# Kernel optimization log

Hardware: AMD Instinct MI355X
Metric: run time of the kernel (lower is better)

## Reference

```python
import jax, jax.numpy as jnp
import numpy as np

N = 50000   # nodes
E = 1000000 # edges
D = 64      # input_nf = output_nf = hidden_nf
COORDS_WEIGHT = 1.0


def setup_inputs() -> dict:
    key = jax.random.key(0)
    ks = jax.random.split(key, 16)
    h = jax.random.normal(ks[0], (N, D), dtype=jnp.float32)
    coord = jax.random.normal(ks[1], (N, 3), dtype=jnp.float32)
    edge_index = jax.random.randint(ks[2], (2, E), 0, N, dtype=jnp.int32)
    s = 0.05  # generic init scale
    # edge_mlp: Linear(2D+1 -> D), ReLU, Linear(D -> D), ReLU
    We1 = jax.random.normal(ks[3], (2 * D + 1, D), dtype=jnp.float32) * s
    be1 = jnp.zeros((D,), dtype=jnp.float32)
    We2 = jax.random.normal(ks[4], (D, D), dtype=jnp.float32) * s
    be2 = jnp.zeros((D,), dtype=jnp.float32)
    # node_mlp: Linear(2D -> D), ReLU, Linear(D -> D)
    Wn1 = jax.random.normal(ks[5], (2 * D, D), dtype=jnp.float32) * s
    bn1 = jnp.zeros((D,), dtype=jnp.float32)
    Wn2 = jax.random.normal(ks[6], (D, D), dtype=jnp.float32) * s
    bn2 = jnp.zeros((D,), dtype=jnp.float32)
    # coord_mlp: Linear(D -> D), ReLU, Linear(D -> 1, no bias, xavier gain 0.001)
    Wc1 = jax.random.normal(ks[7], (D, D), dtype=jnp.float32) * s
    bc1 = jnp.zeros((D,), dtype=jnp.float32)
    Wc2 = jax.random.normal(ks[8], (D, 1), dtype=jnp.float32) * 0.001
    return {"h": h, "coord": coord, "edge_index": edge_index,
            "We1": We1, "be1": be1, "We2": We2, "be2": be2,
            "Wn1": Wn1, "bn1": bn1, "Wn2": Wn2, "bn2": bn2,
            "Wc1": Wc1, "bc1": bc1, "Wc2": Wc2}


def reference(h, coord, edge_index, We1, be1, We2, be2, Wn1, bn1, Wn2, bn2, Wc1, bc1, Wc2):
    row, col = edge_index[0], edge_index[1]
    # coord2radial (no PBC offsets; plain pairwise difference)
    coord_diff = coord[row] - coord[col]                    # [E, 3]
    radial = jnp.sum(coord_diff ** 2, axis=1, keepdims=True)  # [E, 1]

    # edge model: MLP on [h_i, h_j, ||x_i - x_j||^2]
    e_in = jnp.concatenate([h[row], h[col], radial], axis=1)  # [E, 2D+1]
    m = jax.nn.relu(e_in @ We1 + be1)
    edge_feat = jax.nn.relu(m @ We2 + be2)                   # [E, D]

    # coord model: per-edge scalar gate, clamp, segment mean
    gate = jax.nn.relu(edge_feat @ Wc1 + bc1) @ Wc2          # [E, 1]
    trans = jnp.clip(coord_diff * gate, -100.0, 100.0)       # [E, 3]
    trans_sum = jax.ops.segment_sum(trans, row, num_segments=N)  # [N, 3]
    cnt = jax.ops.segment_sum(jnp.ones((row.shape[0],), dtype=trans.dtype), row, num_segments=N)
    coord_out = (trans_sum / jnp.maximum(cnt, 1.0)[:, None]) * COORDS_WEIGHT  # [N, 3]

    # node model: scatter-sum aggregate then MLP with residual
    agg = jax.ops.segment_sum(edge_feat, row, num_segments=N)  # [N, D]
    n_in = jnp.concatenate([h, agg], axis=1)                   # [N, 2D]
    h_out = h + (jax.nn.relu(n_in @ Wn1 + bn1) @ Wn2 + bn2)    # residual
    return (h_out, coord_out)
```

## Files before the change

kernel.cpp:

```cpp
#include <hip/hip_runtime.h>

typedef float  f32x4  __attribute__((ext_vector_type(4)));
typedef __bf16 bf16x8 __attribute__((ext_vector_type(8)));
typedef unsigned short u16x8 __attribute__((ext_vector_type(8)));
typedef unsigned int   u32x4 __attribute__((ext_vector_type(4)));

__device__ inline unsigned short f2b(float f) {
    unsigned u = __builtin_bit_cast(unsigned, f);
    u += 0x7fffu + ((u >> 16) & 1u);
    return (unsigned short)(u >> 16);
}

__device__ inline unsigned pk2(float a, float b) {
    return (unsigned)f2b(a) | ((unsigned)f2b(b) << 16);
}

__device__ inline f32x4 mfma16(bf16x8 a, bf16x8 b, f32x4 c) {
    return __builtin_amdgcn_mfma_f32_16x16x32_bf16(a, b, c, 0, 0, 0);
}

__device__ inline bf16x8 cvt8(f32x4 a, f32x4 b) {
    u16x8 v;
    v[0] = f2b(a[0]); v[1] = f2b(a[1]); v[2] = f2b(a[2]); v[3] = f2b(a[3]);
    v[4] = f2b(b[0]); v[5] = f2b(b[1]); v[6] = f2b(b[2]); v[7] = f2b(b[3]);
    return __builtin_bit_cast(bf16x8, v);
}

__device__ inline bf16x8 ldsA(const unsigned short* base, int frag, int lane) {
    return __builtin_bit_cast(bf16x8,
        *reinterpret_cast<const u16x8*>(base + ((frag * 64 + lane) << 3)));
}

__device__ inline void atom_pk(unsigned short* p, unsigned d) {
    asm volatile("global_atomic_pk_add_bf16 %0, %1, off" :: "v"(p), "v"(d) : "memory");
}

__global__ void k_hist(const int* __restrict__ erow, int* __restrict__ cnt, int E)
{
    int i = blockIdx.x * 256 + threadIdx.x;
    if (i < E) atomicAdd(&cnt[erow[i]], 1);
}

__global__ void k_scan1(const int* __restrict__ cnt, int* __restrict__ bsum, int N)
{
    const int b = blockIdx.x, t = threadIdx.x;
    const int chunk = (N + gridDim.x - 1) / gridDim.x;
    const int lo = b * chunk;
    const int hi = min(lo + chunk, N);
    int s = 0;
    for (int i = lo + t; i < hi; i += 256) s += cnt[i];
#pragma unroll
    for (int d = 1; d < 64; d <<= 1) s += __shfl_xor(s, d, 64);
    __shared__ int ws[4];
    if ((t & 63) == 0) ws[t >> 6] = s;
    __syncthreads();
    if (t == 0) bsum[b] = ws[0] + ws[1] + ws[2] + ws[3];
}

__global__ void k_scan2(int* __restrict__ bsum)
{
    __shared__ int wt[2];
    const int t = threadIdx.x;
    const int lane = t & 63;
    int v = bsum[t];
    int sc = v;
#pragma unroll
    for (int d = 1; d < 64; d <<= 1) { int u = __shfl_up(sc, d, 64); if (lane >= d) sc += u; }
    if (lane == 63) wt[t >> 6] = sc;
    __syncthreads();
    int add = (t >= 64) ? wt[0] : 0;
    bsum[t] = sc - v + add;
}

__global__ void k_scan3(const int* __restrict__ cnt, const int* __restrict__ bsum,
                        int* __restrict__ off, int* __restrict__ woff, int N, int E)
{
    const int b = blockIdx.x, t = threadIdx.x;
    const int chunk = (N + gridDim.x - 1) / gridDim.x;
    const int lo = b * chunk;
    const int hi = min(lo + chunk, N);
    const int tchunk = (chunk + 255) / 256;
    const int tlo = lo + t * tchunk;
    const int thi = min(tlo + tchunk, hi);
    int s = 0;
    for (int i = tlo; i < thi; ++i) s += cnt[i];
    const int lane = t & 63, wv = t >> 6;
    int sc = s;
#pragma unroll
    for (int d = 1; d < 64; d <<= 1) { int u = __shfl_up(sc, d, 64); if (lane >= d) sc += u; }
    __shared__ int ws[4];
    if (lane == 63) ws[wv] = sc;
    __syncthreads();
    int wadd = 0;
#pragma unroll
    for (int k = 0; k < 4; ++k) wadd += (k < wv) ? ws[k] : 0;
    int run = bsum[b] + wadd + (sc - s);
    for (int i = tlo; i < thi; ++i) { off[i] = run; woff[i] = run; run += cnt[i]; }
    if (b == 0 && t == 0) off[N] = E;
}

__global__ void k_scatter(const int* __restrict__ erow, const int* __restrict__ ecol,
                          int* __restrict__ woff, unsigned* __restrict__ spack, int E)
{
    int i = blockIdx.x * 256 + threadIdx.x;
    if (i < E) {
        int r = erow[i];
        int pos = atomicAdd(&woff[r], 1);
        spack[pos] = (unsigned)r | ((unsigned)ecol[i] << 16);
    }
}

__global__ __launch_bounds__(512, 2) void egcl_edge_srt(
    const unsigned short* __restrict__ hb,
    const float* __restrict__ coord,
    const unsigned* __restrict__ spack,
    const float* __restrict__ We1, const float* __restrict__ be1,
    const float* __restrict__ We2, const float* __restrict__ be2,
    const float* __restrict__ Wc1, const float* __restrict__ bc1,
    const float* __restrict__ Wc2,
    unsigned short* __restrict__ aggb, float* __restrict__ cacc, int E)
{
    __shared__ __align__(16) unsigned short A1[16 * 512];
    __shared__ __align__(16) unsigned short A2[8 * 512];
    __shared__ __align__(16) unsigned short A3[8 * 512];
    __shared__ __align__(16) float bv[5][64];
    __shared__ __align__(16) unsigned stl[8][34 * 16];

    const int t = threadIdx.x;
    for (int i = t; i < 8192; i += 512) {
        int j = i & 7, lane = (i >> 3) & 63, fi = i >> 9;
        int mt = fi >> 2, ks = fi & 3;
        int in_ch = ks * 32 + ((lane >> 4) << 3) + j;
        int out   = mt * 16 + (lane & 15);
        A1[i] = f2b(We1[in_ch * 64 + out]);
    }
    for (int i = t; i < 4096; i += 512) {
        int j = i & 7, lane = (i >> 3) & 63, fi = i >> 9;
        int mt = fi >> 1, ks = fi & 1;
        int c   = (ks * 2 + (j >> 2)) * 16 + ((lane >> 4) & 3) * 4 + (j & 3);
        int out = mt * 16 + (lane & 15);
        A2[i] = f2b(We2[c * 64 + out]);
        A3[i] = f2b(Wc1[c * 64 + out]);
    }
    if (t < 64) {
        bv[0][t] = be1[t]; bv[1][t] = We1[128 * 64 + t];
        bv[2][t] = be2[t]; bv[3][t] = bc1[t]; bv[4][t] = Wc2[t];
    }
    __syncthreads();

    const int lane = t & 63;
    const int l16 = lane & 15, lq = lane >> 4;
    const int stride = gridDim.x * 8;
    const int wid = (blockIdx.x << 3) + (t >> 6);
    const int ntile = E >> 4;
    const int last = ntile - 1;
    unsigned* st = stl[t >> 6];

    int tile = wid;
    if (tile >= ntile) return;

    int eC = (tile << 4) + l16;
    unsigned pC = spack[eC];
    int rC = (int)(pC & 0xffffu), cC = (int)(pC >> 16);
    u16x8 hr0, hr1, hc0, hc1;
    {
        const u16x8* hr = reinterpret_cast<const u16x8*>(hb + (size_t)rC * 64);
        const u16x8* hc = reinterpret_cast<const u16x8*>(hb + (size_t)cC * 64);
        hr0 = hr[lq]; hr1 = hr[4 + lq]; hc0 = hc[lq]; hc1 = hc[4 + lq];
    }
    float px = 0.f, py = 0.f, pz = 0.f;
    if (lq < 2) {
        int node = (lq == 0) ? rC : cC;
        const float* pp = coord + (size_t)node * 3;
        px = pp[0]; py = pp[1]; pz = pp[2];
    }
    int t1 = tile + stride;
    int tn = (t1 < ntile) ? t1 : last;
    unsigned pN = spack[(tn << 4) + l16];
    int rN = (int)(pN & 0xffffu), cN = (int)(pN >> 16);

    for (; tile < ntile; ) {
        u16x8 nr0, nr1, nc0, nc1;
        {
            const u16x8* hr = reinterpret_cast<const u16x8*>(hb + (size_t)rN * 64);
            const u16x8* hc = reinterpret_cast<const u16x8*>(hb + (size_t)cN * 64);
            nr0 = hr[lq]; nr1 = hr[4 + lq]; nc0 = hc[lq]; nc1 = hc[4 + lq];
        }
        float npx = 0.f, npy = 0.f, npz = 0.f;
        if (lq < 2) {
            int node = (lq == 0) ? rN : cN;
            const float* pp = coord + (size_t)node * 3;
            npx = pp[0]; npy = pp[1]; npz = pp[2];
        }
        int t2 = tile + 2 * stride;
        int t2c = (t2 < ntile) ? t2 : last;
        unsigned pNN = spack[(t2c << 4) + l16];
        int rNN = (int)(pNN & 0xffffu), cNN = (int)(pNN >> 16);

        float prx = __shfl(px, l16, 64), pry = __shfl(py, l16, 64), prz = __shfl(pz, l16, 64);
        float pcx = __shfl(px, 16 + l16, 64), pcy = __shfl(py, 16 + l16, 64), pcz = __shfl(pz, 16 + l16, 64);
        float dx = prx - pcx, dy = pry - pcy, dz = prz - pcz;
        float rad = dx * dx + dy * dy + dz * dz;

        bf16x8 bR[2] = { __builtin_bit_cast(bf16x8, hr0), __builtin_bit_cast(bf16x8, hr1) };
        bf16x8 bC[2] = { __builtin_bit_cast(bf16x8, hc0), __builtin_bit_cast(bf16x8, hc1) };

        f32x4 a1[4];
#pragma unroll
        for (int mt = 0; mt < 4; ++mt)
            a1[mt] = *reinterpret_cast<const f32x4*>(&bv[0][mt * 16 + lq * 4]);
#pragma unroll
        for (int ks = 0; ks < 2; ++ks)
#pragma unroll
            for (int mt = 0; mt < 4; ++mt)
                a1[mt] = mfma16(ldsA(A1, mt * 4 + ks, lane), bR[ks], a1[mt]);
#pragma unroll
        for (int ks = 0; ks < 2; ++ks)
#pragma unroll
            for (int mt = 0; mt < 4; ++mt)
                a1[mt] = mfma16(ldsA(A1, mt * 4 + 2 + ks, lane), bC[ks], a1[mt]);
#pragma unroll
        for (int mt = 0; mt < 4; ++mt) {
            f32x4 wv = *reinterpret_cast<const f32x4*>(&bv[1][mt * 16 + lq * 4]);
#pragma unroll
            for (int rr = 0; rr < 4; ++rr)
                a1[mt][rr] = fmaxf(a1[mt][rr] + rad * wv[rr], 0.f);
        }

        bf16x8 b2[2] = { cvt8(a1[0], a1[1]), cvt8(a1[2], a1[3]) };
        f32x4 a2[4];
#pragma unroll
        for (int mt = 0; mt < 4; ++mt)
            a2[mt] = *reinterpret_cast<const f32x4*>(&bv[2][mt * 16 + lq * 4]);
#pragma unroll
        for (int ks = 0; ks < 2; ++ks)
#pragma unroll
            for (int mt = 0; mt < 4; ++mt)
                a2[mt] = mfma16(ldsA(A2, mt * 2 + ks, lane), b2[ks], a2[mt]);
#pragma unroll
        for (int mt = 0; mt < 4; ++mt)
#pragma unroll
            for (int rr = 0; rr < 4; ++rr)
                a2[mt][rr] = fmaxf(a2[mt][rr], 0.f);

#pragma unroll
        for (int mt = 0; mt < 4; ++mt) {
            int cp0 = mt * 8 + lq * 2;
            int sw  = l16 ^ (cp0 & 12);
            st[(cp0 + 0) * 16 + sw] = pk2(a2[mt][0], a2[mt][1]);
            st[(cp0 + 1) * 16 + sw] = pk2(a2[mt][2], a2[mt][3]);
        }

        bf16x8 b3[2] = { cvt8(a2[0], a2[1]), cvt8(a2[2], a2[3]) };
        f32x4 a3[4];
#pragma unroll
        for (int mt = 0; mt < 4; ++mt)
            a3[mt] = *reinterpret_cast<const f32x4*>(&bv[3][mt * 16 + lq * 4]);
#pragma unroll
        for (int ks = 0; ks < 2; ++ks)
#pragma unroll
            for (int mt = 0; mt < 4; ++mt)
                a3[mt] = mfma16(ldsA(A3, mt * 2 + ks, lane), b3[ks], a3[mt]);
        float gg = 0.f;
#pragma unroll
        for (int mt = 0; mt < 4; ++mt) {
            f32x4 wv = *reinterpret_cast<const f32x4*>(&bv[4][mt * 16 + lq * 4]);
#pragma unroll
            for (int rr = 0; rr < 4; ++rr)
                gg += fmaxf(a3[mt][rr], 0.f) * wv[rr];
        }
        gg += __shfl_xor(gg, 16, 64);
        gg += __shfl_xor(gg, 32, 64);

        float dsel = (lq == 0) ? dx : (lq == 1) ? dy : dz;
        float val  = fminf(fmaxf(dsel * gg, -100.f), 100.f);

        float vy = __shfl(val, 16 + l16, 64);
        if (lq == 0) st[32 * 16 + l16] = pk2(val, vy);
        if (lq == 2) st[33 * 16 + l16] = pk2(val, 1.0f);

        u16x8 sv;
#pragma unroll
        for (int j = 0; j < 8; ++j) {
            int ks = lq * 8 + j;
            int rk = __shfl(rC, ks & 15, 64);
            sv[j] = (ks < 16 && rk == rC) ? (unsigned short)0x3F80 : (unsigned short)0;
        }
        bf16x8 self = __builtin_bit_cast(bf16x8, sv);

        f32x4 pg[5];
#pragma unroll
        for (int k = 0; k < 5; ++k) pg[k] = (f32x4){0.f, 0.f, 0.f, 0.f};
        const int elo = (lq & 1) << 3;
#pragma unroll
        for (int tt = 0; tt < 5; ++tt) {
            int cpb = (tt < 4) ? (tt * 8 + (l16 >> 1)) : (32 + ((l16 >> 1) & 1));
            int c   = cpb & 12;
            u32x4 wa = *reinterpret_cast<const u32x4*>(st + cpb * 16 + (elo ^ c));
            u32x4 wb = *reinterpret_cast<const u32x4*>(st + cpb * 16 + ((elo + 4) ^ c));
            u16x8 av;
#pragma unroll
            for (int j = 0; j < 4; ++j) {
                av[j]     = (l16 & 1) ? (unsigned short)(wa[j] >> 16)
                                      : (unsigned short)(wa[j] & 0xffffu);
                av[4 + j] = (l16 & 1) ? (unsigned short)(wb[j] >> 16)
                                      : (unsigned short)(wb[j] & 0xffffu);
            }
            pg[tt] = mfma16(__builtin_bit_cast(bf16x8, av), self, pg[tt]);
        }

#pragma unroll
        for (int mt = 0; mt < 4; ++mt) {
            int cp0 = mt * 8 + lq * 2;
            int sw  = l16 ^ (cp0 & 12);
            st[(cp0 + 0) * 16 + sw] = pk2(pg[mt][0], pg[mt][1]);
            st[(cp0 + 1) * 16 + sw] = pk2(pg[mt][2], pg[mt][3]);
        }

        int rprev = __shfl(rC, (lane & 48) | ((l16 + 15) & 15), 64);
        bool lead = (l16 == 0) || (rprev != rC);

        if (lead && lq == 0) {
#pragma unroll
            for (int rr = 0; rr < 4; ++rr)
                atomicAdd(&cacc[(size_t)rC * 4 + rr], pg[4][rr]);
        }

        {
            unsigned m = (unsigned)(__ballot(lead) & 0xFFFFull);
            const int cp = lane & 31;
            const int half = lane >> 5;
            while (m) {
                int s0 = __builtin_ctz(m); m &= m - 1;
                int s1 = 16;
                if (m) { s1 = __builtin_ctz(m); m &= m - 1; }
                int s = half ? s1 : s0;
                if (s < 16) {
                    int rw = __shfl(rC, s, 64);
                    unsigned pkd = st[cp * 16 + (s ^ (cp & 12))];
                    atom_pk(aggb + (size_t)rw * 64 + cp * 2, pkd);
                }
            }
        }

        tile = t1; t1 = tile + stride;
        rC = rN; cC = cN; rN = rNN; cN = cNN;
        hr0 = nr0; hr1 = nr1; hc0 = nc0; hc1 = nc1;
        px = npx; py = npy; pz = npz;
    }
}

__global__ __launch_bounds__(512, 4) void egcl_edge_fb(
    const float* __restrict__ h, const float* __restrict__ coord,
    const int* __restrict__ erow, const int* __restrict__ ecol,
    const float* __restrict__ We1, const float* __restrict__ be1,
    const float* __restrict__ We2, const float* __restrict__ be2,
    const float* __restrict__ Wc1, const float* __restrict__ bc1,
    const float* __restrict__ Wc2,
    float* __restrict__ aggf, float* __restrict__ cacc, int E)
{
    __shared__ __align__(16) unsigned short A1[16 * 512];
    __shared__ __align__(16) unsigned short A2[8 * 512];
    __shared__ __align__(16) unsigned short A3[8 * 512];
    __shared__ __align__(16) float bv[5][64];

    const int t = threadIdx.x;
    for (int i = t; i < 8192; i += 512) {
        int j = i & 7, lane = (i >> 3) & 63, fi = i >> 9;
        int mt = fi >> 2, ks = fi & 3;
        int in_ch = ks * 32 + ((lane >> 4) << 3) + j;
        int out   = mt * 16 + (lane & 15);
        A1[i] = f2b(We1[in_ch * 64 + out]);
    }
    for (int i = t; i < 4096; i += 512) {
        int j = i & 7, lane = (i >> 3) & 63, fi = i >> 9;
        int mt = fi >> 1, ks = fi & 1;
        int c   = (ks * 2 + (j >> 2)) * 16 + ((lane >> 4) & 3) * 4 + (j & 3);
        int out = mt * 16 + (lane & 15);
        A2[i] = f2b(We2[c * 64 + out]);
        A3[i] = f2b(Wc1[c * 64 + out]);
    }
    if (t < 64) {
        bv[0][t] = be1[t]; bv[1][t] = We1[128 * 64 + t];
        bv[2][t] = be2[t]; bv[3][t] = bc1[t]; bv[4][t] = Wc2[t];
    }
    __syncthreads();

    const int lane = t & 63;
    const int l16 = lane & 15, lq = lane >> 4;
    const int stride = gridDim.x * 8;
    const int wid = (blockIdx.x << 3) + (t >> 6);
    const int ntile = E >> 4;

    for (int tile = wid; tile < ntile; tile += stride) {
        const int e = (tile << 4) + l16;
        const int r = erow[e], c = ecol[e];
        const float* pr = coord + (size_t)r * 3;
        const float* pc = coord + (size_t)c * 3;
        float dx = pr[0] - pc[0], dy = pr[1] - pc[1], dz = pr[2] - pc[2];
        float rad = dx * dx + dy * dy + dz * dz;
        const f32x4* hr = reinterpret_cast<const f32x4*>(h + (size_t)r * 64);
        const f32x4* hc = reinterpret_cast<const f32x4*>(h + (size_t)c * 64);
        bf16x8 bR[2], bC[2];
#pragma unroll
        for (int ks = 0; ks < 2; ++ks) {
            bR[ks] = cvt8(hr[ks * 8 + lq * 2], hr[ks * 8 + lq * 2 + 1]);
            bC[ks] = cvt8(hc[ks * 8 + lq * 2], hc[ks * 8 + lq * 2 + 1]);
        }
        f32x4 a1[4];
#pragma unroll
        for (int mt = 0; mt < 4; ++mt)
            a1[mt] = *reinterpret_cast<const f32x4*>(&bv[0][mt * 16 + lq * 4]);
#pragma unroll
        for (int ks = 0; ks < 2; ++ks)
#pragma unroll
            for (int mt = 0; mt < 4; ++mt)
                a1[mt] = mfma16(ldsA(A1, mt * 4 + ks, lane), bR[ks], a1[mt]);
#pragma unroll
        for (int ks = 0; ks < 2; ++ks)
#pragma unroll
            for (int mt = 0; mt < 4; ++mt)
                a1[mt] = mfma16(ldsA(A1, mt * 4 + 2 + ks, lane), bC[ks], a1[mt]);
#pragma unroll
        for (int mt = 0; mt < 4; ++mt) {
            f32x4 wv = *reinterpret_cast<const f32x4*>(&bv[1][mt * 16 + lq * 4]);
#pragma unroll
            for (int rr = 0; rr < 4; ++rr)
                a1[mt][rr] = fmaxf(a1[mt][rr] + rad * wv[rr], 0.f);
        }
        bf16x8 b2[2] = { cvt8(a1[0], a1[1]), cvt8(a1[2], a1[3]) };
        f32x4 a2[4];
#pragma unroll
        for (int mt = 0; mt < 4; ++mt)
            a2[mt] = *reinterpret_cast<const f32x4*>(&bv[2][mt * 16 + lq * 4]);
#pragma unroll
        for (int ks = 0; ks < 2; ++ks)
#pragma unroll
            for (int mt = 0; mt < 4; ++mt)
                a2[mt] = mfma16(ldsA(A2, mt * 2 + ks, lane), b2[ks], a2[mt]);
#pragma unroll
        for (int mt = 0; mt < 4; ++mt)
#pragma unroll
            for (int rr = 0; rr < 4; ++rr) {
                a2[mt][rr] = fmaxf(a2[mt][rr], 0.f);
                atomicAdd(&aggf[(size_t)r * 64 + mt * 16 + lq * 4 + rr], a2[mt][rr]);
            }
        bf16x8 b3[2] = { cvt8(a2[0], a2[1]), cvt8(a2[2], a2[3]) };
        f32x4 a3[4];
#pragma unroll
        for (int mt = 0; mt < 4; ++mt)
            a3[mt] = *reinterpret_cast<const f32x4*>(&bv[3][mt * 16 + lq * 4]);
#pragma unroll
        for (int ks = 0; ks < 2; ++ks)
#pragma unroll
            for (int mt = 0; mt < 4; ++mt)
                a3[mt] = mfma16(ldsA(A3, mt * 2 + ks, lane), b3[ks], a3[mt]);
        float gg = 0.f;
#pragma unroll
        for (int mt = 0; mt < 4; ++mt) {
            f32x4 wv = *reinterpret_cast<const f32x4*>(&bv[4][mt * 16 + lq * 4]);
#pragma unroll
            for (int rr = 0; rr < 4; ++rr)
                gg += fmaxf(a3[mt][rr], 0.f) * wv[rr];
        }
        gg += __shfl_xor(gg, 16, 64);
        gg += __shfl_xor(gg, 32, 64);
        float dsel = (lq == 0) ? dx : (lq == 1) ? dy : dz;
        float val  = (lq == 3) ? 1.0f : fminf(fmaxf(dsel * gg, -100.f), 100.f);
        atomicAdd(&cacc[(size_t)r * 4 + lq], val);
    }
}

__device__ inline void stage_wblock(unsigned short* dst, const float* src, int t, int nthr) {
    for (int i = t; i < 4096; i += nthr) {
        int k = i >> 6, n = i & 63;
        int pos = (((n >> 4) * 2 + (k >> 5)) * 64 + ((((k >> 3) & 3) << 4) | (n & 15))) * 8 + (k & 7);
        dst[pos] = f2b(src[i]);
    }
}

__device__ inline bf16x8 ldsB(const unsigned short* base, int nt, int ks, int lane) {
    return __builtin_bit_cast(bf16x8,
        *reinterpret_cast<const u16x8*>(base + (((nt * 2 + ks) * 64 + lane) << 3)));
}

template<bool PK>
__global__ __launch_bounds__(256) void egcl_node(
    const float* __restrict__ h, const unsigned short* __restrict__ hb,
    const float* __restrict__ aggf, const unsigned short* __restrict__ aggb,
    const float* __restrict__ Wn1, const float* __restrict__ bn1,
    const float* __restrict__ Wn2, const float* __restrict__ bn2,
    float* __restrict__ hout, int N)
{
    __shared__ __align__(16) unsigned short wlds[3][4096];
    __shared__ __align__(16) unsigned short mlds[4][16 * 72];
    __shared__ float bn1l[64], bn2l[64];

    const int t = threadIdx.x;
    stage_wblock(wlds[0], Wn1, t, 256);
    stage_wblock(wlds[1], Wn1 + 64 * 64, t, 256);
    stage_wblock(wlds[2], Wn2, t, 256);
    if (t < 64) { bn1l[t] = bn1[t]; bn2l[t] = bn2[t]; }
    __syncthreads();

    const int wave = t >> 6, lane = t & 63;
    const int l16 = lane & 15, lq = lane >> 4;
    const int ntile = N >> 4;
    unsigned short* ml = mlds[wave];

    for (int tile = blockIdx.x * 4 + wave; tile < ntile; tile += gridDim.x * 4) {
        const int nb = tile << 4;
        bf16x8 fH[2], fA[2];
        if constexpr (PK) {
            const u16x8* ph = reinterpret_cast<const u16x8*>(hb + (size_t)(nb + l16) * 64);
            const u16x8* pa = reinterpret_cast<const u16x8*>(aggb + (size_t)(nb + l16) * 64);
#pragma unroll
            for (int ks = 0; ks < 2; ++ks) {
                fH[ks] = __builtin_bit_cast(bf16x8, ph[ks * 4 + lq]);
                fA[ks] = __builtin_bit_cast(bf16x8, pa[ks * 4 + lq]);
            }
        } else {
            const f32x4* ph = reinterpret_cast<const f32x4*>(h + (size_t)(nb + l16) * 64);
            const f32x4* pa = reinterpret_cast<const f32x4*>(aggf + (size_t)(nb + l16) * 64);
#pragma unroll
            for (int ks = 0; ks < 2; ++ks) {
                fH[ks] = cvt8(ph[ks * 8 + lq * 2], ph[ks * 8 + lq * 2 + 1]);
                fA[ks] = cvt8(pa[ks * 8 + lq * 2], pa[ks * 8 + lq * 2 + 1]);
            }
        }
        f32x4 acc[4];
#pragma unroll
        for (int nt = 0; nt < 4; ++nt) { float b = bn1l[nt * 16 + l16]; acc[nt] = (f32x4){b, b, b, b}; }
#pragma unroll
        for (int ks = 0; ks < 2; ++ks)
#pragma unroll
            for (int nt = 0; nt < 4; ++nt)
                acc[nt] = mfma16(fH[ks], ldsB(wlds[0], nt, ks, lane), acc[nt]);
#pragma unroll
        for (int ks = 0; ks < 2; ++ks)
#pragma unroll
            for (int nt = 0; nt < 4; ++nt)
                acc[nt] = mfma16(fA[ks], ldsB(wlds[1], nt, ks, lane), acc[nt]);
#pragma unroll
        for (int nt = 0; nt < 4; ++nt)
#pragma unroll
            for (int r = 0; r < 4; ++r)
                ml[(lq * 4 + r) * 72 + nt * 16 + l16] = f2b(fmaxf(acc[nt][r], 0.f));
        bf16x8 fM[2];
#pragma unroll
        for (int ks = 0; ks < 2; ++ks)
            fM[ks] = __builtin_bit_cast(bf16x8,
                *reinterpret_cast<const u16x8*>(ml + l16 * 72 + ks * 32 + lq * 8));
        f32x4 acc2[4];
#pragma unroll
        for (int nt = 0; nt < 4; ++nt) { float b = bn2l[nt * 16 + l16]; acc2[nt] = (f32x4){b, b, b, b}; }
#pragma unroll
        for (int ks = 0; ks < 2; ++ks)
#pragma unroll
            for (int nt = 0; nt < 4; ++nt)
                acc2[nt] = mfma16(fM[ks], ldsB(wlds[2], nt, ks, lane), acc2[nt]);
#pragma unroll
        for (int nt = 0; nt < 4; ++nt)
#pragma unroll
            for (int r = 0; r < 4; ++r) {
                size_t idx = (size_t)(nb + lq * 4 + r) * 64 + nt * 16 + l16;
                hout[idx] = h[idx] + acc2[nt][r];
            }
    }
}

__global__ void f32_to_bf16(const float* __restrict__ src, unsigned short* __restrict__ dst, int n8)
{
    int i = blockIdx.x * 256 + threadIdx.x;
    if (i < n8) {
        const f32x4* p = reinterpret_cast<const f32x4*>(src + (size_t)i * 8);
        bf16x8 v = cvt8(p[0], p[1]);
        reinterpret_cast<u16x8*>(dst)[i] = __builtin_bit_cast(u16x8, v);
    }
}

__global__ void egcl_coord(const float* __restrict__ cacc, float* __restrict__ cout, int N)
{
    int n = blockIdx.x * 256 + threadIdx.x;
    if (n < N) {
        f32x4 c = *reinterpret_cast<const f32x4*>(cacc + (size_t)n * 4);
        float inv = 1.f / fmaxf(c[3], 1.f);
        cout[n * 3 + 0] = c[0] * inv;
        cout[n * 3 + 1] = c[1] * inv;
        cout[n * 3 + 2] = c[2] * inv;
    }
}

extern "C" void kernel_launch(void* const* d_in, const int* in_sizes, int n_in,
                              void* d_out, int out_size, void* d_ws, size_t ws_size,
                              hipStream_t stream)
{
    const float* h     = (const float*)d_in[0];
    const float* coord = (const float*)d_in[1];
    const int*   eidx  = (const int*)d_in[2];
    const float* We1 = (const float*)d_in[3];  const float* be1 = (const float*)d_in[4];
    const float* We2 = (const float*)d_in[5];  const float* be2 = (const float*)d_in[6];
    const float* Wn1 = (const float*)d_in[7];  const float* bn1 = (const float*)d_in[8];
    const float* Wn2 = (const float*)d_in[9];  const float* bn2 = (const float*)d_in[10];
    const float* Wc1 = (const float*)d_in[11]; const float* bc1 = (const float*)d_in[12];
    const float* Wc2 = (const float*)d_in[13];

    const int N = in_sizes[0] / 64;
    const int E = in_sizes[2] / 2;

    float* hout = (float*)d_out;
    float* cout = hout + (size_t)N * 64;

    const int ntileN = N >> 4;
    const int nblkN  = (ntileN + 3) / 4;

    int*      cnt   = (int*)d_ws;
    int*      off   = (int*)((char*)d_ws + (256u << 10));
    int*      woff  = (int*)((char*)d_ws + (512u << 10));
    int*      bsum  = (int*)((char*)d_ws + (768u << 10));
    float*    cacc  = (float*)d_ws;
    unsigned* spack = (unsigned*)((char*)d_ws + (1u << 20));
    unsigned short* hb   = (unsigned short*)((char*)d_ws + (5u << 20));
    unsigned short* aggb = (unsigned short*)((char*)d_ws + (12u << 20));

    const size_t need_sorted = (12u << 20) + (size_t)N * 128;
    const bool use_sorted = (ws_size >= need_sorted) && N > 0 && (N % 16 == 0)
                            && (N <= 65536) && (E % 16 == 0)
                            && ((size_t)E * 4 <= (4u << 20));

    if (use_sorted) {
        hipMemsetAsync(cnt, 0, (size_t)N * sizeof(int), stream);
        int n8 = N * 8;
        f32_to_bf16<<<(n8 + 255) / 256, 256, 0, stream>>>(h, hb, n8);
        k_hist<<<(E + 255) / 256, 256, 0, stream>>>(eidx, cnt, E);
        k_scan1<<<128, 256, 0, stream>>>(cnt, bsum, N);
        k_scan2<<<1, 128, 0, stream>>>(bsum);
        k_scan3<<<128, 256, 0, stream>>>(cnt, bsum, off, woff, N, E);
        k_scatter<<<(E + 255) / 256, 256, 0, stream>>>(eidx, eidx + E, woff, spack, E);
        hipMemsetAsync(cacc, 0, (size_t)N * 4 * sizeof(float), stream);
        hipMemsetAsync(aggb, 0, (size_t)N * 128, stream);
        egcl_edge_srt<<<2048, 512, 0, stream>>>(hb, coord, spack,
                                                We1, be1, We2, be2, Wc1, bc1, Wc2,
                                                aggb, cacc, E);
        egcl_node<true><<<nblkN, 256, 0, stream>>>(h, hb, nullptr, aggb,
                                                   Wn1, bn1, Wn2, bn2, hout, N);
        egcl_coord<<<(N + 255) / 256, 256, 0, stream>>>(cacc, cout, N);
    } else {
        float* aggf = hout;
        hipMemsetAsync(cacc, 0, (size_t)N * 4 * sizeof(float), stream);
        hipMemsetAsync(aggf, 0, (size_t)N * 64 * sizeof(float), stream);
        egcl_edge_fb<<<2048, 512, 0, stream>>>(h, coord, eidx, eidx + E,
                                               We1, be1, We2, be2, Wc1, bc1, Wc2,
                                               aggf, cacc, E);
        egcl_node<false><<<nblkN, 256, 0, stream>>>(h, nullptr, aggf, nullptr,
                                                    Wn1, bn1, Wn2, bn2, hout, N);
        egcl_coord<<<(N + 255) / 256, 256, 0, stream>>>(cacc, cout, N);
    }
}
```

Baseline: 247.7 us.

## Fuse preprocessing kernels, single-block scan, hardware bf16 packing, fold coord finalize

Merges the f32-to-bf16 conversion, the aggb zeroing and the row histogram into one prep kernel. It replaces the three-pass multi-block prefix scan with one 1024-thread block, and folds the cacc zeroing into the scatter kernel. The coord-mean finalize moves into the node kernel, which now launches a fixed 256-block grid. Software bf16 rounding is replaced by the v_cvt_pk_bf16_f32 instruction. The aim is to cut kernel launches, memsets and ALU work, at the risk of a slower serial single-block scan and reliance on the node kernel looping over all tiles with the smaller grid.

```diff
diff --git a/kernel.cpp b/kernel.cpp
--- a/kernel.cpp
+++ b/kernel.cpp
@@ -11,8 +11,10 @@
     return (unsigned short)(u >> 16);
 }
 
-__device__ inline unsigned pk2(float a, float b) {
-    return (unsigned)f2b(a) | ((unsigned)f2b(b) << 16);
+__device__ inline unsigned cvtpk(float a, float b) {
+    unsigned r;
+    asm("v_cvt_pk_bf16_f32 %0, %1, %2" : "=v"(r) : "v"(a), "v"(b));
+    return r;
 }
 
 __device__ inline f32x4 mfma16(bf16x8 a, bf16x8 b, f32x4 c) {
@@ -20,10 +22,10 @@
 }
 
 __device__ inline bf16x8 cvt8(f32x4 a, f32x4 b) {
-    u16x8 v;
-    v[0] = f2b(a[0]); v[1] = f2b(a[1]); v[2] = f2b(a[2]); v[3] = f2b(a[3]);
-    v[4] = f2b(b[0]); v[5] = f2b(b[1]); v[6] = f2b(b[2]); v[7] = f2b(b[3]);
-    return __builtin_bit_cast(bf16x8, v);
+    u32x4 w;
+    w[0] = cvtpk(a[0], a[1]); w[1] = cvtpk(a[2], a[3]);
+    w[2] = cvtpk(b[0], b[1]); w[3] = cvtpk(b[2], b[3]);
+    return __builtin_bit_cast(bf16x8, w);
 }
 
 __device__ inline bf16x8 ldsA(const unsigned short* base, int frag, int lane) {
@@ -35,74 +37,61 @@
     asm volatile("global_atomic_pk_add_bf16 %0, %1, off" :: "v"(p), "v"(d) : "memory");
 }
 
-__global__ void k_hist(const int* __restrict__ erow, int* __restrict__ cnt, int E)
+__global__ void k_prep(const float* __restrict__ h, unsigned short* __restrict__ hb,
+                       u16x8* __restrict__ aggb8,
+                       const int* __restrict__ erow, int* __restrict__ cnt,
+                       int n8, int E)
 {
     int i = blockIdx.x * 256 + threadIdx.x;
+    if (i < n8) {
+        const f32x4* p = reinterpret_cast<const f32x4*>(h + (size_t)i * 8);
+        bf16x8 v = cvt8(p[0], p[1]);
+        reinterpret_cast<u16x8*>(hb)[i] = __builtin_bit_cast(u16x8, v);
+        aggb8[i] = (u16x8){0, 0, 0, 0, 0, 0, 0, 0};
+    }
     if (i < E) atomicAdd(&cnt[erow[i]], 1);
 }
 
-__global__ void k_scan1(const int* __restrict__ cnt, int* __restrict__ bsum, int N)
-{
-    const int b = blockIdx.x, t = threadIdx.x;
-    const int chunk = (N + gridDim.x - 1) / gridDim.x;
-    const int lo = b * chunk;
-    const int hi = min(lo + chunk, N);
+__global__ void k_scan(const int* __restrict__ cnt, int* __restrict__ woff, int N)
+{
+    __shared__ int wsum[16];
+    const int t = threadIdx.x;
+    const int lane = t & 63, w = t >> 6;
+    const int chunk = (N + 1023) >> 10;
+    const int lo = t * chunk;
+    const int hi = (lo + chunk < N) ? lo + chunk : N;
     int s = 0;
-    for (int i = lo + t; i < hi; i += 256) s += cnt[i];
-#pragma unroll
-    for (int d = 1; d < 64; d <<= 1) s += __shfl_xor(s, d, 64);
-    __shared__ int ws[4];
-    if ((t & 63) == 0) ws[t >> 6] = s;
+    for (int i = lo; i < hi; ++i) s += cnt[i];
+    int sc = s;
+#pragma unroll
+    for (int d = 1; d < 64; d <<= 1) {
+        int v = __shfl_up(sc, d, 64);
+        if (lane >= d) sc += v;
+    }
+    if (lane == 63) wsum[w] = sc;
     __syncthreads();
-    if (t == 0) bsum[b] = ws[0] + ws[1] + ws[2] + ws[3];
-}
-
-__global__ void k_scan2(int* __restrict__ bsum)
-{
-    __shared__ int wt[2];
-    const int t = threadIdx.x;
-    const int lane = t & 63;
-    int v = bsum[t];
-    int sc = v;
-#pragma unroll
-    for (int d = 1; d < 64; d <<= 1) { int u = __shfl_up(sc, d, 64); if (lane >= d) sc += u; }
-    if (lane == 63) wt[t >> 6] = sc;
+    if (w == 0 && lane < 16) {
+        int v = wsum[lane];
+        int scw = v;
+#pragma unroll
+        for (int d = 1; d < 16; d <<= 1) {
+            int u = __shfl_up(scw, d, 16);
+            if (lane >= d) scw += u;
+        }
+        wsum[lane] = scw - v;
+    }
     __syncthreads();
-    int add = (t >= 64) ? wt[0] : 0;
-    bsum[t] = sc - v + add;
-}
-
-__global__ void k_scan3(const int* __restrict__ cnt, const int* __restrict__ bsum,
-                        int* __restrict__ off, int* __restrict__ woff, int N, int E)
-{
-    const int b = blockIdx.x, t = threadIdx.x;
-    const int chunk = (N + gridDim.x - 1) / gridDim.x;
-    const int lo = b * chunk;
-    const int hi = min(lo + chunk, N);
-    const int tchunk = (chunk + 255) / 256;
-    const int tlo = lo + t * tchunk;
-    const int thi = min(tlo + tchunk, hi);
-    int s = 0;
-    for (int i = tlo; i < thi; ++i) s += cnt[i];
-    const int lane = t & 63, wv = t >> 6;
-    int sc = s;
-#pragma unroll
-    for (int d = 1; d < 64; d <<= 1) { int u = __shfl_up(sc, d, 64); if (lane >= d) sc += u; }
-    __shared__ int ws[4];
-    if (lane == 63) ws[wv] = sc;
-    __syncthreads();
-    int wadd = 0;
-#pragma unroll
-    for (int k = 0; k < 4; ++k) wadd += (k < wv) ? ws[k] : 0;
-    int run = bsum[b] + wadd + (sc - s);
-    for (int i = tlo; i < thi; ++i) { off[i] = run; woff[i] = run; run += cnt[i]; }
-    if (b == 0 && t == 0) off[N] = E;
+    int run = wsum[w] + (sc - s);
+    for (int i = lo; i < hi; ++i) { woff[i] = run; run += cnt[i]; }
 }
 
 __global__ void k_scatter(const int* __restrict__ erow, const int* __restrict__ ecol,
-                          int* __restrict__ woff, unsigned* __restrict__ spack, int E)
+                          int* __restrict__ woff, unsigned* __restrict__ spack,
+                          float* __restrict__ cacc, int N, int E)
 {
     int i = blockIdx.x * 256 + threadIdx.x;
+    if (i < N)
+        *reinterpret_cast<f32x4*>(cacc + (size_t)i * 4) = (f32x4){0.f, 0.f, 0.f, 0.f};
     if (i < E) {
         int r = erow[i];
         int pos = atomicAdd(&woff[r], 1);
@@ -247,8 +236,8 @@
         for (int mt = 0; mt < 4; ++mt) {
             int cp0 = mt * 8 + lq * 2;
             int sw  = l16 ^ (cp0 & 12);
-            st[(cp0 + 0) * 16 + sw] = pk2(a2[mt][0], a2[mt][1]);
-            st[(cp0 + 1) * 16 + sw] = pk2(a2[mt][2], a2[mt][3]);
+            st[(cp0 + 0) * 16 + sw] = cvtpk(a2[mt][0], a2[mt][1]);
+            st[(cp0 + 1) * 16 + sw] = cvtpk(a2[mt][2], a2[mt][3]);
         }
 
         bf16x8 b3[2] = { cvt8(a2[0], a2[1]), cvt8(a2[2], a2[3]) };
@@ -276,8 +265,8 @@
         float val  = fminf(fmaxf(dsel * gg, -100.f), 100.f);
 
         float vy = __shfl(val, 16 + l16, 64);
-        if (lq == 0) st[32 * 16 + l16] = pk2(val, vy);
-        if (lq == 2) st[33 * 16 + l16] = pk2(val, 1.0f);
+        if (lq == 0) st[32 * 16 + l16] = cvtpk(val, vy);
+        if (lq == 2) st[33 * 16 + l16] = cvtpk(val, 1.0f);
 
         u16x8 sv;
 #pragma unroll
@@ -313,8 +302,8 @@
         for (int mt = 0; mt < 4; ++mt) {
             int cp0 = mt * 8 + lq * 2;
             int sw  = l16 ^ (cp0 & 12);
-            st[(cp0 + 0) * 16 + sw] = pk2(pg[mt][0], pg[mt][1]);
-            st[(cp0 + 1) * 16 + sw] = pk2(pg[mt][2], pg[mt][3]);
+            st[(cp0 + 0) * 16 + sw] = cvtpk(pg[mt][0], pg[mt][1]);
+            st[(cp0 + 1) * 16 + sw] = cvtpk(pg[mt][2], pg[mt][3]);
         }
 
         int rprev = __shfl(rC, (lane & 48) | ((l16 + 15) & 15), 64);
@@ -490,6 +479,7 @@
     const float* __restrict__ aggf, const unsigned short* __restrict__ aggb,
     const float* __restrict__ Wn1, const float* __restrict__ bn1,
     const float* __restrict__ Wn2, const float* __restrict__ bn2,
+    const float* __restrict__ cacc, float* __restrict__ cout,
     float* __restrict__ hout, int N)
 {
     __shared__ __align__(16) unsigned short wlds[3][4096];
@@ -566,16 +556,15 @@
                 size_t idx = (size_t)(nb + lq * 4 + r) * 64 + nt * 16 + l16;
                 hout[idx] = h[idx] + acc2[nt][r];
             }
-    }
-}
-
-__global__ void f32_to_bf16(const float* __restrict__ src, unsigned short* __restrict__ dst, int n8)
-{
-    int i = blockIdx.x * 256 + threadIdx.x;
-    if (i < n8) {
-        const f32x4* p = reinterpret_cast<const f32x4*>(src + (size_t)i * 8);
-        bf16x8 v = cvt8(p[0], p[1]);
-        reinterpret_cast<u16x8*>(dst)[i] = __builtin_bit_cast(u16x8, v);
+        if constexpr (PK) {
+            if (lq == 0) {
+                f32x4 cc = *reinterpret_cast<const f32x4*>(cacc + (size_t)(nb + l16) * 4);
+                float inv = 1.f / fmaxf(cc[3], 1.f);
+                cout[(size_t)(nb + l16) * 3 + 0] = cc[0] * inv;
+                cout[(size_t)(nb + l16) * 3 + 1] = cc[1] * inv;
+                cout[(size_t)(nb + l16) * 3 + 2] = cc[2] * inv;
+            }
+        }
     }
 }
 
@@ -615,10 +604,8 @@
     const int nblkN  = (ntileN + 3) / 4;
 
     int*      cnt   = (int*)d_ws;
-    int*      off   = (int*)((char*)d_ws + (256u << 10));
-    int*      woff  = (int*)((char*)d_ws + (512u << 10));
-    int*      bsum  = (int*)((char*)d_ws + (768u << 10));
     float*    cacc  = (float*)d_ws;
+    int*      woff  = (int*)((char*)d_ws + (800u << 10));
     unsigned* spack = (unsigned*)((char*)d_ws + (1u << 20));
     unsigned short* hb   = (unsigned short*)((char*)d_ws + (5u << 20));
     unsigned short* aggb = (unsigned short*)((char*)d_ws + (12u << 20));
@@ -629,22 +616,16 @@
                             && ((size_t)E * 4 <= (4u << 20));
 
     if (use_sorted) {
+        const int n8 = N * 8;
         hipMemsetAsync(cnt, 0, (size_t)N * sizeof(int), stream);
-        int n8 = N * 8;
-        f32_to_bf16<<<(n8 + 255) / 256, 256, 0, stream>>>(h, hb, n8);
-        k_hist<<<(E + 255) / 256, 256, 0, stream>>>(eidx, cnt, E);
-        k_scan1<<<128, 256, 0, stream>>>(cnt, bsum, N);
-        k_scan2<<<1, 128, 0, stream>>>(bsum);
-        k_scan3<<<128, 256, 0, stream>>>(cnt, bsum, off, woff, N, E);
-        k_scatter<<<(E + 255) / 256, 256, 0, stream>>>(eidx, eidx + E, woff, spack, E);
-        hipMemsetAsync(cacc, 0, (size_t)N * 4 * sizeof(float), stream);
-        hipMemsetAsync(aggb, 0, (size_t)N * 128, stream);
+        k_prep<<<(E + 255) / 256, 256, 0, stream>>>(h, hb, (u16x8*)aggb, eidx, cnt, n8, E);
+        k_scan<<<1, 1024, 0, stream>>>(cnt, woff, N);
+        k_scatter<<<(E + 255) / 256, 256, 0, stream>>>(eidx, eidx + E, woff, spack, cacc, N, E);
         egcl_edge_srt<<<2048, 512, 0, stream>>>(hb, coord, spack,
                                                 We1, be1, We2, be2, Wc1, bc1, Wc2,
                                                 aggb, cacc, E);
-        egcl_node<true><<<nblkN, 256, 0, stream>>>(h, hb, nullptr, aggb,
-                                                   Wn1, bn1, Wn2, bn2, hout, N);
-        egcl_coord<<<(N + 255) / 256, 256, 0, stream>>>(cacc, cout, N);
+        egcl_node<true><<<256, 256, 0, stream>>>(h, hb, nullptr, aggb,
+                                                 Wn1, bn1, Wn2, bn2, cacc, cout, hout, N);
     } else {
         float* aggf = hout;
         hipMemsetAsync(cacc, 0, (size_t)N * 4 * sizeof(float), stream);
@@ -653,7 +634,7 @@
                                                We1, be1, We2, be2, Wc1, bc1, Wc2,
                                                aggf, cacc, E);
         egcl_node<false><<<nblkN, 256, 0, stream>>>(h, nullptr, aggf, nullptr,
-                                                    Wn1, bn1, Wn2, bn2, hout, N);
+                                                    Wn1, bn1, Wn2, bn2, nullptr, nullptr, hout, N);
         egcl_coord<<<(N + 255) / 256, 256, 0, stream>>>(cacc, cout, N);
     }
 }
```

Measured after the change: 297.4 us. 20.1% more time.
